# Kernel tuning notes

Measured on AMD Instinct MI355X. Metric: run time of the kernel, lower is better.

The kernel has to match this reference:

```python
import jax, jax.numpy as jnp
import numpy as np

NUM_HEADS = 32
HEAD_DIM = 128
HIDDEN = 4096
MAX_SEQ = 4096
B, S = 8, 16
POS = 2048


def setup_inputs() -> dict:
    key = jax.random.key(0)
    ks = jax.random.split(key, 7)
    sc = 1.0 / np.sqrt(HIDDEN)
    return {
        "h": jax.random.normal(ks[0], (B, S, HIDDEN), dtype=jnp.float32),
        "Wq": jax.random.normal(ks[1], (HIDDEN, HIDDEN), dtype=jnp.float32) * sc,
        "Wk": jax.random.normal(ks[2], (HIDDEN, HIDDEN), dtype=jnp.float32) * sc,
        "Wv": jax.random.normal(ks[3], (HIDDEN, HIDDEN), dtype=jnp.float32) * sc,
        "Wo": jax.random.normal(ks[4], (HIDDEN, HIDDEN), dtype=jnp.float32) * sc,
        "K_cache": jax.random.normal(ks[5], (B, NUM_HEADS, MAX_SEQ, HEAD_DIM), dtype=jnp.float32),
        "V_cache": jax.random.normal(ks[6], (B, NUM_HEADS, MAX_SEQ, HEAD_DIM), dtype=jnp.float32),
        "pos": POS,
    }


def reference(h, Wq, Wk, Wv, Wo, K_cache, V_cache, pos):
    b, s, _ = h.shape
    # QKV projections (Linear with weight [out, in], no bias): h @ W.T
    def proj(W):
        return (h @ W.T).reshape(b, s, NUM_HEADS, HEAD_DIM).transpose(0, 2, 1, 3)  # [B,H,S,hd]
    Q, K, V = proj(Wq), proj(Wk), proj(Wv)
    # write new K/V into cache at [pos : pos+S] (pos is a static Python int)
    K_cache = K_cache.at[:, :, pos:pos + s, :].set(K)
    V_cache = V_cache.at[:, :, pos:pos + s, :].set(V)
    K_all = K_cache[:, :, :pos + s, :]  # [B,H,T,hd], T = pos+S
    V_all = V_cache[:, :, :pos + s, :]
    scores = jnp.einsum('bhsd,bhtd->bhst', Q, K_all) / np.sqrt(HEAD_DIM)  # [B,H,S,T]
    if s > 1:
        # causal mask applied only to the freshly-written block of columns
        causal = jnp.triu(jnp.full((s, s), -jnp.inf, dtype=scores.dtype), k=1)
        scores = scores.at[:, :, :, pos:pos + s].add(causal)
    attn = jax.nn.softmax(scores, axis=-1)
    out = jnp.einsum('bhst,bhtd->bhsd', attn, V_all)  # [B,H,S,hd]
    out = out.transpose(0, 2, 1, 3).reshape(b, s, NUM_HEADS * HEAD_DIM)
    return out @ Wo.T
```

## Files before the change

kernel.cpp:

```cpp
#include <hip/hip_runtime.h>

typedef _Float16 f16;
typedef _Float16 f16x8 __attribute__((ext_vector_type(8)));
typedef _Float16 f16x4 __attribute__((ext_vector_type(4)));
typedef _Float16 f16x2 __attribute__((ext_vector_type(2)));
typedef float f32x4 __attribute__((ext_vector_type(4)));
typedef float f32x2 __attribute__((ext_vector_type(2)));

#define MFMA16(a, b, c) __builtin_amdgcn_mfma_f32_16x16x32_f16(a, b, c, 0, 0, 0)

#define HID 4096
#define ROWS 128
#define SCL 0.12751743f

__device__ __forceinline__ f16x8 cvt8(float4 x, float4 y) {
    f16x8 v = {(f16)x.x, (f16)x.y, (f16)x.z, (f16)x.w,
               (f16)y.x, (f16)y.y, (f16)y.z, (f16)y.w};
    return v;
}

__device__ __forceinline__ int swz2(int row, int cb) {
    return row * 256 + (cb ^ ((row & 7) << 4));
}

__global__ void k_cvt(const float* __restrict__ src, f16* __restrict__ dst) {
    const int i = blockIdx.x * blockDim.x + threadIdx.x;
    const float4* s4 = (const float4*)src + (size_t)i * 2;
    float4 x = s4[0], y = s4[1];
    *((f16x8*)dst + i) = cvt8(x, y);
}

__global__ __launch_bounds__(256) void k_proj(
        const f16* __restrict__ hb,
        const float* __restrict__ Wq, const float* __restrict__ Wk,
        const float* __restrict__ Wv,
        f16* __restrict__ Qw, f16* __restrict__ Kw, f16* __restrict__ Vw) {
    const int mat = blockIdx.x >> 8;
    const int ct  = blockIdx.x & 255;
    const float* __restrict__ W = (mat == 0) ? Wq : (mat == 1) ? Wk : Wv;
    f16* __restrict__ Ob = (mat == 0) ? Qw : (mat == 1) ? Kw : Vw;
    const int c0 = ct * 16;

    __shared__ __align__(16) f16 sA[128 * 128];
    __shared__ __align__(16) f16 sB[16 * 128];

    const int tid = threadIdx.x;
    const int w = tid >> 6, l = tid & 63;
    const int rw = w * 32;
    const int ar = tid >> 4;
    const int ac = (tid & 15) * 8;

    f32x4 acc0 = {}, acc1 = {};

    float4 wx, wy;
    f16x8 hreg[8];
    {
        const float* wp = W + (size_t)(c0 + ar) * HID + ac;
        wx = *(const float4*)wp; wy = *(const float4*)(wp + 4);
        #pragma unroll
        for (int c = 0; c < 8; ++c)
            hreg[c] = *(const f16x8*)(hb + (size_t)(c * 16 + ar) * HID + ac);
    }

    for (int ks = 0; ks < 32; ++ks) {
        #pragma unroll
        for (int c = 0; c < 8; ++c)
            *(f16x8*)((char*)sA + swz2(c * 16 + ar, ac * 2)) = hreg[c];
        *(f16x8*)((char*)sB + swz2(ar, ac * 2)) = cvt8(wx, wy);
        __syncthreads();
        if (ks < 31) {
            const int k0 = (ks + 1) * 128;
            const float* wp = W + (size_t)(c0 + ar) * HID + k0 + ac;
            wx = *(const float4*)wp; wy = *(const float4*)(wp + 4);
            #pragma unroll
            for (int c = 0; c < 8; ++c)
                hreg[c] = *(const f16x8*)(hb + (size_t)(c * 16 + ar) * HID + k0 + ac);
        }
        #pragma unroll
        for (int kk = 0; kk < 4; ++kk) {
            const int cb = kk * 64 + (l >> 4) * 16;
            f16x8 a0 = *(const f16x8*)((char*)sA + swz2(rw + (l & 15), cb));
            f16x8 a1 = *(const f16x8*)((char*)sA + swz2(rw + 16 + (l & 15), cb));
            f16x8 b0 = *(const f16x8*)((char*)sB + swz2((l & 15), cb));
            acc0 = MFMA16(a0, b0, acc0);
            acc1 = MFMA16(a1, b0, acc1);
        }
        __syncthreads();
    }
    #pragma unroll
    for (int r = 0; r < 4; ++r) {
        const int col = c0 + (l & 15);
        Ob[(size_t)(rw + (l >> 4) * 4 + r) * HID + col]      = (f16)acc0[r];
        Ob[(size_t)(rw + 16 + (l >> 4) * 4 + r) * HID + col] = (f16)acc1[r];
    }
}

__global__ __launch_bounds__(512) void k_attn(
        const f16* __restrict__ Qw, const f16* __restrict__ Kw,
        const f16* __restrict__ Vw,
        const float* __restrict__ Kc, const float* __restrict__ Vc,
        const int* __restrict__ posp, f16* __restrict__ Ow) {

    __shared__ __align__(16) char smem[65536 + 1024];

    const int bh = blockIdx.x;
    const int b = bh >> 5, hh = bh & 31;
    const int tid = threadIdx.x, w = tid >> 6, l = tid & 63;
    const int pos = *posp;
    const int npure = pos >> 5;

    const float* Kb = Kc + (size_t)bh * (4096 * 128);
    const float* Vb = Vc + (size_t)bh * (4096 * 128);

    f16x8 qf[4];
    {
        const f16* qp = Qw + (size_t)(b * 16 + (l & 15)) * HID + hh * 128 + (l >> 4) * 8;
        #pragma unroll
        for (int kk = 0; kk < 4; ++kk) qf[kk] = *(const f16x8*)(qp + kk * 32);
    }

    f32x4 o[8] = {};
    float m[4], lsum[4];
    #pragma unroll
    for (int r = 0; r < 4; ++r) { m[r] = -3e38f; lsum[r] = 0.f; }

    f16* Pw = (f16*)smem + w * 640;

    const int start = (w * npure) >> 3;
    const int end   = ((w + 1) * npure) >> 3;
    for (int tau = start; tau < end; ++tau) {
        const int t0 = tau << 5;

        f16x8 kf[2][4];
        #pragma unroll
        for (int tn = 0; tn < 2; ++tn) {
            const float* kp = Kb + (size_t)(t0 + tn * 16 + (l & 15)) * 128 + (l >> 4) * 8;
            #pragma unroll
            for (int kk = 0; kk < 4; ++kk) {
                float4 x = *(const float4*)(kp + kk * 32);
                float4 y = *(const float4*)(kp + kk * 32 + 4);
                kf[tn][kk] = cvt8(x, y);
            }
        }
        f32x4 sa[2] = {};
        #pragma unroll
        for (int tn = 0; tn < 2; ++tn)
            #pragma unroll
            for (int kk = 0; kk < 4; ++kk) sa[tn] = MFMA16(qf[kk], kf[tn][kk], sa[tn]);

        f16x8 vf[8];
        {
            const float* vp = Vb + (size_t)(t0 + (l >> 4) * 8) * 128 + (l & 15);
            #pragma unroll
            for (int dt = 0; dt < 8; ++dt)
                #pragma unroll
                for (int j = 0; j < 8; ++j) vf[dt][j] = (f16)vp[j * 128 + dt * 16];
        }

        float sc[2][4];
        #pragma unroll
        for (int tn = 0; tn < 2; ++tn)
            #pragma unroll
            for (int r = 0; r < 4; ++r) sc[tn][r] = sa[tn][r] * SCL;
        float vmax[4];
        #pragma unroll
        for (int r = 0; r < 4; ++r) vmax[r] = fmaxf(sc[0][r], sc[1][r]);
        #pragma unroll
        for (int d = 1; d < 16; d <<= 1)
            #pragma unroll
            for (int r = 0; r < 4; ++r) vmax[r] = fmaxf(vmax[r], __shfl_xor(vmax[r], d));
        float p[2][4], rs[4], fac[4];
        #pragma unroll
        for (int r = 0; r < 4; ++r) {
            const float mn = fmaxf(m[r], vmax[r]);
            fac[r] = exp2f(m[r] - mn);
            m[r] = mn;
            p[0][r] = exp2f(sc[0][r] - mn);
            p[1][r] = exp2f(sc[1][r] - mn);
            rs[r] = p[0][r] + p[1][r];
            lsum[r] *= fac[r];
        }
        #pragma unroll
        for (int d = 1; d < 16; d <<= 1)
            #pragma unroll
            for (int r = 0; r < 4; ++r) rs[r] += __shfl_xor(rs[r], d);
        #pragma unroll
        for (int r = 0; r < 4; ++r) lsum[r] += rs[r];
        #pragma unroll
        for (int dt = 0; dt < 8; ++dt)
            #pragma unroll
            for (int r = 0; r < 4; ++r) o[dt][r] *= fac[r];

        #pragma unroll
        for (int r = 0; r < 4; ++r) {
            const int s_ = (l >> 4) * 4 + r;
            Pw[s_ * 40 + (l & 15)]      = (f16)p[0][r];
            Pw[s_ * 40 + 16 + (l & 15)] = (f16)p[1][r];
        }
        asm volatile("s_waitcnt lgkmcnt(0)" ::: "memory");
        f16x8 pa = *(const f16x8*)(Pw + (l & 15) * 40 + (l >> 4) * 8);

        #pragma unroll
        for (int dt = 0; dt < 8; ++dt) o[dt] = MFMA16(pa, vf[dt], o[dt]);
    }

    if (w == 7) {
        for (int t0 = npure << 5; t0 < pos + 16; t0 += 32) {
            f32x4 sa[2] = {};
            bool tnv[2];
            #pragma unroll
            for (int tn = 0; tn < 2; ++tn) {
                tnv[tn] = (t0 + tn * 16 < pos + 16);
                if (!tnv[tn]) continue;
                const int trow = t0 + tn * 16 + (l & 15);
                f16x8 kf[4];
                if (trow < pos) {
                    const float* kp = Kb + (size_t)trow * 128 + (l >> 4) * 8;
                    #pragma unroll
                    for (int kk = 0; kk < 4; ++kk) {
                        float4 x = *(const float4*)(kp + kk * 32);
                        float4 y = *(const float4*)(kp + kk * 32 + 4);
                        kf[kk] = cvt8(x, y);
                    }
                } else {
                    const int tt = trow - pos;
                    const int rr = tt < 15 ? tt : 15;
                    const f16* kp = Kw + (size_t)(b * 16 + rr) * HID + hh * 128 + (l >> 4) * 8;
                    #pragma unroll
                    for (int kk = 0; kk < 4; ++kk) kf[kk] = *(const f16x8*)(kp + kk * 32);
                }
                #pragma unroll
                for (int kk = 0; kk < 4; ++kk) sa[tn] = MFMA16(qf[kk], kf[kk], sa[tn]);
            }

            float sc[2][4];
            #pragma unroll
            for (int tn = 0; tn < 2; ++tn) {
                const int tg = t0 + tn * 16 + (l & 15);
                #pragma unroll
                for (int r = 0; r < 4; ++r) {
                    if (!tnv[tn]) { sc[tn][r] = -3e38f; continue; }
                    float v = sa[tn][r] * SCL;
                    if (tg >= pos) {
                        const int tt = tg - pos;
                        const int s_ = (l >> 4) * 4 + r;
                        if (tt > s_ || tt >= 16) v = -3e38f;
                    }
                    sc[tn][r] = v;
                }
            }

            float vmax[4];
            #pragma unroll
            for (int r = 0; r < 4; ++r) vmax[r] = fmaxf(sc[0][r], sc[1][r]);
            #pragma unroll
            for (int d = 1; d < 16; d <<= 1)
                #pragma unroll
                for (int r = 0; r < 4; ++r) vmax[r] = fmaxf(vmax[r], __shfl_xor(vmax[r], d));
            float p[2][4], rs[4], fac[4];
            #pragma unroll
            for (int r = 0; r < 4; ++r) {
                const float mn = fmaxf(m[r], vmax[r]);
                fac[r] = exp2f(m[r] - mn);
                m[r] = mn;
                p[0][r] = sc[0][r] < -1e29f ? 0.f : exp2f(sc[0][r] - mn);
                p[1][r] = sc[1][r] < -1e29f ? 0.f : exp2f(sc[1][r] - mn);
                rs[r] = p[0][r] + p[1][r];
                lsum[r] *= fac[r];
            }
            #pragma unroll
            for (int d = 1; d < 16; d <<= 1)
                #pragma unroll
                for (int r = 0; r < 4; ++r) rs[r] += __shfl_xor(rs[r], d);
            #pragma unroll
            for (int r = 0; r < 4; ++r) lsum[r] += rs[r];
            #pragma unroll
            for (int dt = 0; dt < 8; ++dt)
                #pragma unroll
                for (int r = 0; r < 4; ++r) o[dt][r] *= fac[r];

            #pragma unroll
            for (int r = 0; r < 4; ++r) {
                const int s_ = (l >> 4) * 4 + r;
                Pw[s_ * 40 + (l & 15)]      = (f16)p[0][r];
                Pw[s_ * 40 + 16 + (l & 15)] = (f16)p[1][r];
            }
            asm volatile("s_waitcnt lgkmcnt(0)" ::: "memory");
            f16x8 pa = *(const f16x8*)(Pw + (l & 15) * 40 + (l >> 4) * 8);

            const int tb = t0 + (l >> 4) * 8;
            #pragma unroll
            for (int dt = 0; dt < 8; ++dt) {
                f16x8 vf;
                #pragma unroll
                for (int j = 0; j < 8; ++j) {
                    const int t = tb + j;
                    if (t < pos) {
                        vf[j] = (f16)Vb[(size_t)t * 128 + dt * 16 + (l & 15)];
                    } else {
                        const int rr = (t - pos < 15) ? (t - pos) : 15;
                        vf[j] = Vw[(size_t)(b * 16 + rr) * HID + hh * 128 + dt * 16 + (l & 15)];
                    }
                }
                o[dt] = MFMA16(pa, vf, o[dt]);
            }
        }
    }

    __syncthreads();
    float* Osh = (float*)smem;
    float* Msh = (float*)(smem + 65536);
    float* Lsh = Msh + 128;
    #pragma unroll
    for (int dt = 0; dt < 8; ++dt)
        #pragma unroll
        for (int r = 0; r < 4; ++r)
            Osh[w * 2048 + ((l >> 4) * 4 + r) * 128 + dt * 16 + (l & 15)] = o[dt][r];
    if ((l & 15) == 0) {
        #pragma unroll
        for (int r = 0; r < 4; ++r) {
            Msh[w * 16 + (l >> 4) * 4 + r] = m[r];
            Lsh[w * 16 + (l >> 4) * 4 + r] = lsum[r];
        }
    }
    __syncthreads();
    {
        const int s_ = tid >> 5;
        const int d_ = (tid & 31) * 4;
        float M = -3e38f;
        #pragma unroll
        for (int ww = 0; ww < 8; ++ww) M = fmaxf(M, Msh[ww * 16 + s_]);
        float L = 0.f;
        f32x4 oa = {};
        #pragma unroll
        for (int ww = 0; ww < 8; ++ww) {
            const float e = exp2f(Msh[ww * 16 + s_] - M);
            L += e * Lsh[ww * 16 + s_];
            f32x4 v = *(const f32x4*)(Osh + ww * 2048 + s_ * 128 + d_);
            #pragma unroll
            for (int r = 0; r < 4; ++r) oa[r] += e * v[r];
        }
        const float inv = 1.f / L;
        f16x4 res = {(f16)(oa[0] * inv), (f16)(oa[1] * inv),
                     (f16)(oa[2] * inv), (f16)(oa[3] * inv)};
        *(f16x4*)(Ow + (size_t)(b * 16 + s_) * HID + hh * 128 + d_) = res;
    }
}

__global__ __launch_bounds__(256) void k_oproj(
        const f16* __restrict__ Oa, const float* __restrict__ Wo,
        float* __restrict__ out) {
    const int c0 = blockIdx.x * 16;

    __shared__ __align__(16) f16 sA[128 * 128];
    __shared__ __align__(16) f16 sB[16 * 128];

    const int tid = threadIdx.x;
    const int w = tid >> 6, l = tid & 63;
    const int rw = w * 32;
    const int ar = tid >> 4;
    const int ac = (tid & 15) * 8;

    f32x4 acc0 = {}, acc1 = {};

    float4 wx, wy;
    f16x8 hreg[8];
    {
        const float* wp = Wo + (size_t)(c0 + ar) * HID + ac;
        wx = *(const float4*)wp; wy = *(const float4*)(wp + 4);
        #pragma unroll
        for (int c = 0; c < 8; ++c)
            hreg[c] = *(const f16x8*)(Oa + (size_t)(c * 16 + ar) * HID + ac);
    }

    for (int ks = 0; ks < 32; ++ks) {
        #pragma unroll
        for (int c = 0; c < 8; ++c)
            *(f16x8*)((char*)sA + swz2(c * 16 + ar, ac * 2)) = hreg[c];
        *(f16x8*)((char*)sB + swz2(ar, ac * 2)) = cvt8(wx, wy);
        __syncthreads();
        if (ks < 31) {
            const int k0 = (ks + 1) * 128;
            const float* wp = Wo + (size_t)(c0 + ar) * HID + k0 + ac;
            wx = *(const float4*)wp; wy = *(const float4*)(wp + 4);
            #pragma unroll
            for (int c = 0; c < 8; ++c)
                hreg[c] = *(const f16x8*)(Oa + (size_t)(c * 16 + ar) * HID + k0 + ac);
        }
        #pragma unroll
        for (int kk = 0; kk < 4; ++kk) {
            const int cb = kk * 64 + (l >> 4) * 16;
            f16x8 a0 = *(const f16x8*)((char*)sA + swz2(rw + (l & 15), cb));
            f16x8 a1 = *(const f16x8*)((char*)sA + swz2(rw + 16 + (l & 15), cb));
            f16x8 b0 = *(const f16x8*)((char*)sB + swz2((l & 15), cb));
            acc0 = MFMA16(a0, b0, acc0);
            acc1 = MFMA16(a1, b0, acc1);
        }
        __syncthreads();
    }
    #pragma unroll
    for (int r = 0; r < 4; ++r) {
        const int col = c0 + (l & 15);
        out[(size_t)(rw + (l >> 4) * 4 + r) * HID + col]      = acc0[r];
        out[(size_t)(rw + 16 + (l >> 4) * 4 + r) * HID + col] = acc1[r];
    }
}

extern "C" void kernel_launch(void* const* d_in, const int* in_sizes, int n_in,
                              void* d_out, int out_size, void* d_ws, size_t ws_size,
                              hipStream_t stream) {
    const float* h  = (const float*)d_in[0];
    const float* Wq = (const float*)d_in[1];
    const float* Wk = (const float*)d_in[2];
    const float* Wv = (const float*)d_in[3];
    const float* Wo = (const float*)d_in[4];
    const float* Kc = (const float*)d_in[5];
    const float* Vc = (const float*)d_in[6];
    const int* pos  = (const int*)d_in[7];
    float* out = (float*)d_out;

    f16* hws = (f16*)d_ws;
    f16* Qw  = hws + ROWS * HID;
    f16* Kw  = Qw + ROWS * HID;
    f16* Vw  = Kw + ROWS * HID;
    f16* Ow  = Vw + ROWS * HID;

    k_cvt<<<256, 256, 0, stream>>>(h, hws);
    k_proj<<<768, 256, 0, stream>>>(hws, Wq, Wk, Wv, Qw, Kw, Vw);
    k_attn<<<256, 512, 0, stream>>>(Qw, Kw, Vw, Kc, Vc, pos, Ow);
    k_oproj<<<256, 256, 0, stream>>>(Ow, Wo, out);
}
```

Before: 205.6 us.

## Overlap K/V projection with cached-prefix attention in one interleaved kernel

The Q projection now runs on its own. The K and V projections are merged into one launch with the attention over the pure cached prefix: odd blocks do the K/V GEMM and even blocks compute partial softmax state (max, sum, output) for each head. A new finalize kernel then handles the tail block, including the newly written K/V rows, with the causal mask, and merges it with the partial results. This is meant to hide the long cache-streaming attention behind the projection GEMM and to remove the slow single-wave tail loop. The cost is an extra launch and a round trip of the partial results through global memory.

```diff
diff --git a/kernel.cpp b/kernel.cpp
--- a/kernel.cpp
+++ b/kernel.cpp
@@ -30,16 +30,10 @@
     *((f16x8*)dst + i) = cvt8(x, y);
 }
 
-__global__ __launch_bounds__(256) void k_proj(
-        const f16* __restrict__ hb,
-        const float* __restrict__ Wq, const float* __restrict__ Wk,
-        const float* __restrict__ Wv,
-        f16* __restrict__ Qw, f16* __restrict__ Kw, f16* __restrict__ Vw) {
-    const int mat = blockIdx.x >> 8;
-    const int ct  = blockIdx.x & 255;
-    const float* __restrict__ W = (mat == 0) ? Wq : (mat == 1) ? Wk : Wv;
-    f16* __restrict__ Ob = (mat == 0) ? Qw : (mat == 1) ? Kw : Vw;
-    const int c0 = ct * 16;
+__global__ __launch_bounds__(256) void k_qproj(
+        const f16* __restrict__ hb, const float* __restrict__ W,
+        f16* __restrict__ Ob) {
+    const int c0 = blockIdx.x * 16;
 
     __shared__ __align__(16) f16 sA[128 * 128];
     __shared__ __align__(16) f16 sB[16 * 128];
@@ -95,17 +89,81 @@
     }
 }
 
-__global__ __launch_bounds__(512) void k_attn(
-        const f16* __restrict__ Qw, const f16* __restrict__ Kw,
-        const f16* __restrict__ Vw,
+__global__ __launch_bounds__(512) void k_mega(
+        const f16* __restrict__ hb,
+        const float* __restrict__ Wk, const float* __restrict__ Wv,
+        f16* __restrict__ Kw, f16* __restrict__ Vw,
+        const f16* __restrict__ Qw,
         const float* __restrict__ Kc, const float* __restrict__ Vc,
-        const int* __restrict__ posp, f16* __restrict__ Ow) {
+        const int* __restrict__ posp,
+        float* __restrict__ Pm, float* __restrict__ Pl, float* __restrict__ Po) {
 
     __shared__ __align__(16) char smem[65536 + 1024];
-
-    const int bh = blockIdx.x;
+    const int tid = threadIdx.x, w = tid >> 6, l = tid & 63;
+
+    if (blockIdx.x & 1) {
+        const int pid = blockIdx.x >> 1;
+        const float* __restrict__ W = (pid & 128) ? Wv : Wk;
+        f16* __restrict__ Ob = (pid & 128) ? Vw : Kw;
+        const int c0 = (pid & 127) * 32;
+
+        f16* sA = (f16*)smem;
+        f16* sB = (f16*)smem + 128 * 128;
+
+        const int ar = tid >> 4;
+        const int ac = (tid & 15) * 8;
+
+        f32x4 acc0 = {}, acc1 = {};
+
+        float4 wx, wy;
+        f16x8 hreg[4];
+        {
+            const float* wp = W + (size_t)(c0 + ar) * HID + ac;
+            wx = *(const float4*)wp; wy = *(const float4*)(wp + 4);
+            #pragma unroll
+            for (int c = 0; c < 4; ++c)
+                hreg[c] = *(const f16x8*)(hb + (size_t)(c * 32 + ar) * HID + ac);
+        }
+
+        const int rw = (w >> 1) * 32;
+        const int cw = (w & 1) * 16;
+
+        for (int ks = 0; ks < 32; ++ks) {
+            #pragma unroll
+            for (int c = 0; c < 4; ++c)
+                *(f16x8*)((char*)sA + swz2(c * 32 + ar, ac * 2)) = hreg[c];
+            *(f16x8*)((char*)sB + swz2(ar, ac * 2)) = cvt8(wx, wy);
+            __syncthreads();
+            if (ks < 31) {
+                const int k0 = (ks + 1) * 128;
+                const float* wp = W + (size_t)(c0 + ar) * HID + k0 + ac;
+                wx = *(const float4*)wp; wy = *(const float4*)(wp + 4);
+                #pragma unroll
+                for (int c = 0; c < 4; ++c)
+                    hreg[c] = *(const f16x8*)(hb + (size_t)(c * 32 + ar) * HID + k0 + ac);
+            }
+            #pragma unroll
+            for (int kk = 0; kk < 4; ++kk) {
+                const int cb = kk * 64 + (l >> 4) * 16;
+                f16x8 a0 = *(const f16x8*)((char*)sA + swz2(rw + (l & 15), cb));
+                f16x8 a1 = *(const f16x8*)((char*)sA + swz2(rw + 16 + (l & 15), cb));
+                f16x8 b0 = *(const f16x8*)((char*)sB + swz2(cw + (l & 15), cb));
+                acc0 = MFMA16(a0, b0, acc0);
+                acc1 = MFMA16(a1, b0, acc1);
+            }
+            __syncthreads();
+        }
+        #pragma unroll
+        for (int r = 0; r < 4; ++r) {
+            const int col = c0 + cw + (l & 15);
+            Ob[(size_t)(rw + (l >> 4) * 4 + r) * HID + col]      = (f16)acc0[r];
+            Ob[(size_t)(rw + 16 + (l >> 4) * 4 + r) * HID + col] = (f16)acc1[r];
+        }
+        return;
+    }
+
+    const int bh = blockIdx.x >> 1;
     const int b = bh >> 5, hh = bh & 31;
-    const int tid = threadIdx.x, w = tid >> 6, l = tid & 63;
     const int pos = *posp;
     const int npure = pos >> 5;
 
@@ -204,109 +262,6 @@
         for (int dt = 0; dt < 8; ++dt) o[dt] = MFMA16(pa, vf[dt], o[dt]);
     }
 
-    if (w == 7) {
-        for (int t0 = npure << 5; t0 < pos + 16; t0 += 32) {
-            f32x4 sa[2] = {};
-            bool tnv[2];
-            #pragma unroll
-            for (int tn = 0; tn < 2; ++tn) {
-                tnv[tn] = (t0 + tn * 16 < pos + 16);
-                if (!tnv[tn]) continue;
-                const int trow = t0 + tn * 16 + (l & 15);
-                f16x8 kf[4];
-                if (trow < pos) {
-                    const float* kp = Kb + (size_t)trow * 128 + (l >> 4) * 8;
-                    #pragma unroll
-                    for (int kk = 0; kk < 4; ++kk) {
-                        float4 x = *(const float4*)(kp + kk * 32);
-                        float4 y = *(const float4*)(kp + kk * 32 + 4);
-                        kf[kk] = cvt8(x, y);
-                    }
-                } else {
-                    const int tt = trow - pos;
-                    const int rr = tt < 15 ? tt : 15;
-                    const f16* kp = Kw + (size_t)(b * 16 + rr) * HID + hh * 128 + (l >> 4) * 8;
-                    #pragma unroll
-                    for (int kk = 0; kk < 4; ++kk) kf[kk] = *(const f16x8*)(kp + kk * 32);
-                }
-                #pragma unroll
-                for (int kk = 0; kk < 4; ++kk) sa[tn] = MFMA16(qf[kk], kf[kk], sa[tn]);
-            }
-
-            float sc[2][4];
-            #pragma unroll
-            for (int tn = 0; tn < 2; ++tn) {
-                const int tg = t0 + tn * 16 + (l & 15);
-                #pragma unroll
-                for (int r = 0; r < 4; ++r) {
-                    if (!tnv[tn]) { sc[tn][r] = -3e38f; continue; }
-                    float v = sa[tn][r] * SCL;
-                    if (tg >= pos) {
-                        const int tt = tg - pos;
-                        const int s_ = (l >> 4) * 4 + r;
-                        if (tt > s_ || tt >= 16) v = -3e38f;
-                    }
-                    sc[tn][r] = v;
-                }
-            }
-
-            float vmax[4];
-            #pragma unroll
-            for (int r = 0; r < 4; ++r) vmax[r] = fmaxf(sc[0][r], sc[1][r]);
-            #pragma unroll
-            for (int d = 1; d < 16; d <<= 1)
-                #pragma unroll
-                for (int r = 0; r < 4; ++r) vmax[r] = fmaxf(vmax[r], __shfl_xor(vmax[r], d));
-            float p[2][4], rs[4], fac[4];
-            #pragma unroll
-            for (int r = 0; r < 4; ++r) {
-                const float mn = fmaxf(m[r], vmax[r]);
-                fac[r] = exp2f(m[r] - mn);
-                m[r] = mn;
-                p[0][r] = sc[0][r] < -1e29f ? 0.f : exp2f(sc[0][r] - mn);
-                p[1][r] = sc[1][r] < -1e29f ? 0.f : exp2f(sc[1][r] - mn);
-                rs[r] = p[0][r] + p[1][r];
-                lsum[r] *= fac[r];
-            }
-            #pragma unroll
-            for (int d = 1; d < 16; d <<= 1)
-                #pragma unroll
-                for (int r = 0; r < 4; ++r) rs[r] += __shfl_xor(rs[r], d);
-            #pragma unroll
-            for (int r = 0; r < 4; ++r) lsum[r] += rs[r];
-            #pragma unroll
-            for (int dt = 0; dt < 8; ++dt)
-                #pragma unroll
-                for (int r = 0; r < 4; ++r) o[dt][r] *= fac[r];
-
-            #pragma unroll
-            for (int r = 0; r < 4; ++r) {
-                const int s_ = (l >> 4) * 4 + r;
-                Pw[s_ * 40 + (l & 15)]      = (f16)p[0][r];
-                Pw[s_ * 40 + 16 + (l & 15)] = (f16)p[1][r];
-            }
-            asm volatile("s_waitcnt lgkmcnt(0)" ::: "memory");
-            f16x8 pa = *(const f16x8*)(Pw + (l & 15) * 40 + (l >> 4) * 8);
-
-            const int tb = t0 + (l >> 4) * 8;
-            #pragma unroll
-            for (int dt = 0; dt < 8; ++dt) {
-                f16x8 vf;
-                #pragma unroll
-                for (int j = 0; j < 8; ++j) {
-                    const int t = tb + j;
-                    if (t < pos) {
-                        vf[j] = (f16)Vb[(size_t)t * 128 + dt * 16 + (l & 15)];
-                    } else {
-                        const int rr = (t - pos < 15) ? (t - pos) : 15;
-                        vf[j] = Vw[(size_t)(b * 16 + rr) * HID + hh * 128 + dt * 16 + (l & 15)];
-                    }
-                }
-                o[dt] = MFMA16(pa, vf, o[dt]);
-            }
-        }
-    }
-
     __syncthreads();
     float* Osh = (float*)smem;
     float* Msh = (float*)(smem + 65536);
@@ -340,10 +295,129 @@
             #pragma unroll
             for (int r = 0; r < 4; ++r) oa[r] += e * v[r];
         }
-        const float inv = 1.f / L;
-        f16x4 res = {(f16)(oa[0] * inv), (f16)(oa[1] * inv),
-                     (f16)(oa[2] * inv), (f16)(oa[3] * inv)};
-        *(f16x4*)(Ow + (size_t)(b * 16 + s_) * HID + hh * 128 + d_) = res;
+        if ((tid & 31) == 0) {
+            Pm[bh * 16 + s_] = M;
+            Pl[bh * 16 + s_] = L;
+        }
+        *(f32x4*)(Po + (size_t)bh * 2048 + s_ * 128 + d_) = oa;
+    }
+}
+
+__global__ __launch_bounds__(256) void k_fin(
+        const f16* __restrict__ Qw, const f16* __restrict__ Kw,
+        const f16* __restrict__ Vw,
+        const float* __restrict__ Kc, const float* __restrict__ Vc,
+        const int* __restrict__ posp,
+        const float* __restrict__ Pm, const float* __restrict__ Pl,
+        const float* __restrict__ Po, f16* __restrict__ Ow) {
+
+    __shared__ float sP[16][48];
+    __shared__ float sF[16], sL[16];
+
+    const int bh = blockIdx.x, b = bh >> 5, hh = bh & 31;
+    const int tid = threadIdx.x;
+    const int pos = *posp;
+    const int base = (pos >> 5) << 5;
+    const int nb = pos + 16 - base;
+
+    {
+        const int s_ = tid >> 4, tt0 = tid & 15;
+        const f16* qp = Qw + (size_t)(b * 16 + s_) * HID + hh * 128;
+        const float m_p = Pm[bh * 16 + s_];
+        const float l_p = Pl[bh * 16 + s_];
+
+        float sc[3];
+        float rowmax = -3e38f;
+        #pragma unroll
+        for (int it = 0; it < 3; ++it) {
+            const int tt = it * 16 + tt0;
+            float d = -3e38f;
+            if (tt < nb) {
+                const int t = base + tt;
+                float acc = 0.f;
+                if (t < pos) {
+                    const float* kp = Kc + ((size_t)bh * 4096 + t) * 128;
+                    #pragma unroll
+                    for (int c = 0; c < 16; ++c) {
+                        f16x8 q8 = *(const f16x8*)(qp + c * 8);
+                        float4 ka = *(const float4*)(kp + c * 8);
+                        float4 kb = *(const float4*)(kp + c * 8 + 4);
+                        acc += (float)q8[0] * ka.x + (float)q8[1] * ka.y +
+                               (float)q8[2] * ka.z + (float)q8[3] * ka.w +
+                               (float)q8[4] * kb.x + (float)q8[5] * kb.y +
+                               (float)q8[6] * kb.z + (float)q8[7] * kb.w;
+                    }
+                    d = acc * SCL;
+                } else {
+                    const f16* kp = Kw + (size_t)(b * 16 + (t - pos)) * HID + hh * 128;
+                    #pragma unroll
+                    for (int c = 0; c < 16; ++c) {
+                        f16x8 q8 = *(const f16x8*)(qp + c * 8);
+                        f16x8 k8 = *(const f16x8*)(kp + c * 8);
+                        #pragma unroll
+                        for (int j = 0; j < 8; ++j) acc += (float)q8[j] * (float)k8[j];
+                    }
+                    d = acc * SCL;
+                    if ((t - pos) > s_) d = -3e38f;
+                }
+            }
+            sc[it] = d;
+            rowmax = fmaxf(rowmax, d);
+        }
+        #pragma unroll
+        for (int dd = 1; dd < 16; dd <<= 1)
+            rowmax = fmaxf(rowmax, __shfl_xor(rowmax, dd));
+
+        const float M = fmaxf(m_p, rowmax);
+        const float fac = exp2f(m_p - M);
+        float ps = 0.f;
+        #pragma unroll
+        for (int it = 0; it < 3; ++it) {
+            const float p = (sc[it] < -1e29f) ? 0.f : exp2f(sc[it] - M);
+            ps += p;
+            sP[s_][it * 16 + tt0] = p;
+        }
+        #pragma unroll
+        for (int dd = 1; dd < 16; dd <<= 1) ps += __shfl_xor(ps, dd);
+        if (tt0 == 0) {
+            sF[s_] = fac;
+            sL[s_] = fac * l_p + ps;
+        }
+    }
+    __syncthreads();
+
+    {
+        const int s2 = tid >> 4;
+        const int d0 = (tid & 15) * 8;
+        const float f = sF[s2];
+        float acc[8];
+        const float* po = Po + (size_t)bh * 2048 + s2 * 128 + d0;
+        #pragma unroll
+        for (int j = 0; j < 8; ++j) acc[j] = f * po[j];
+
+        for (int tt = 0; tt < nb; ++tt) {
+            const float pv = sP[s2][tt];
+            const int t = base + tt;
+            if (t < pos) {
+                const float* vp = Vc + ((size_t)bh * 4096 + t) * 128 + d0;
+                float4 va = *(const float4*)vp;
+                float4 vb = *(const float4*)(vp + 4);
+                acc[0] += pv * va.x; acc[1] += pv * va.y;
+                acc[2] += pv * va.z; acc[3] += pv * va.w;
+                acc[4] += pv * vb.x; acc[5] += pv * vb.y;
+                acc[6] += pv * vb.z; acc[7] += pv * vb.w;
+            } else {
+                const f16* vp = Vw + (size_t)(b * 16 + (t - pos)) * HID + hh * 128 + d0;
+                f16x8 v8 = *(const f16x8*)vp;
+                #pragma unroll
+                for (int j = 0; j < 8; ++j) acc[j] += pv * (float)v8[j];
+            }
+        }
+        const float inv = 1.f / sL[s2];
+        f16x8 res;
+        #pragma unroll
+        for (int j = 0; j < 8; ++j) res[j] = (f16)(acc[j] * inv);
+        *(f16x8*)(Ow + (size_t)(b * 16 + s2) * HID + hh * 128 + d0) = res;
     }
 }
 
@@ -424,9 +498,13 @@
     f16* Kw  = Qw + ROWS * HID;
     f16* Vw  = Kw + ROWS * HID;
     f16* Ow  = Vw + ROWS * HID;
+    float* Pm = (float*)(Ow + ROWS * HID);
+    float* Pl = Pm + 256 * 16;
+    float* Po = Pl + 256 * 16;
 
     k_cvt<<<256, 256, 0, stream>>>(h, hws);
-    k_proj<<<768, 256, 0, stream>>>(hws, Wq, Wk, Wv, Qw, Kw, Vw);
-    k_attn<<<256, 512, 0, stream>>>(Qw, Kw, Vw, Kc, Vc, pos, Ow);
+    k_qproj<<<256, 256, 0, stream>>>(hws, Wq, Qw);
+    k_mega<<<512, 512, 0, stream>>>(hws, Wk, Wv, Kw, Vw, Qw, Kc, Vc, pos, Pm, Pl, Po);
+    k_fin<<<256, 256, 0, stream>>>(Qw, Kw, Vw, Kc, Vc, pos, Pm, Pl, Po, Ow);
     k_oproj<<<256, 256, 0, stream>>>(Ow, Wo, out);
 }
```

Measured after the change: 229.1 us. 1.11x slower.

## Load projection MFMA operands directly from global memory, dropping LDS staging

Applied to the files above, without the earlier changes.

The QKV projection kernel no longer stages the activation and weight tiles through shared memory with swizzling and two barriers per k-step. Each lane now loads its MFMA operand fragments straight from global memory into registers, double-buffered across k-steps, and converts weights to fp16 in registers. Launch bounds now request 3 blocks per CU. This removes LDS traffic and synchronization, but each of the four waves independently reloads the same 16-column weight slice, and the per-lane global loads are strided rather than fully coalesced.

```diff
diff --git a/kernel.cpp b/kernel.cpp
--- a/kernel.cpp
+++ b/kernel.cpp
@@ -30,7 +30,7 @@
     *((f16x8*)dst + i) = cvt8(x, y);
 }
 
-__global__ __launch_bounds__(256) void k_proj(
+__global__ __launch_bounds__(256, 3) void k_proj(
         const f16* __restrict__ hb,
         const float* __restrict__ Wq, const float* __restrict__ Wk,
         const float* __restrict__ Wv,
@@ -41,57 +41,61 @@
     f16* __restrict__ Ob = (mat == 0) ? Qw : (mat == 1) ? Kw : Vw;
     const int c0 = ct * 16;
 
-    __shared__ __align__(16) f16 sA[128 * 128];
-    __shared__ __align__(16) f16 sB[16 * 128];
-
     const int tid = threadIdx.x;
     const int w = tid >> 6, l = tid & 63;
-    const int rw = w * 32;
-    const int ar = tid >> 4;
-    const int ac = (tid & 15) * 8;
+    const int r0 = w * 32;
+
+    const float* wp  = W  + (size_t)(c0 + (l & 15)) * HID + ((l >> 4) * 8);
+    const f16*   hp0 = hb + (size_t)(r0 + (l & 15)) * HID + ((l >> 4) * 8);
+    const f16*   hp1 = hp0 + (size_t)16 * HID;
 
     f32x4 acc0 = {}, acc1 = {};
 
-    float4 wx, wy;
-    f16x8 hreg[8];
-    {
-        const float* wp = W + (size_t)(c0 + ar) * HID + ac;
-        wx = *(const float4*)wp; wy = *(const float4*)(wp + 4);
-        #pragma unroll
-        for (int c = 0; c < 8; ++c)
-            hreg[c] = *(const f16x8*)(hb + (size_t)(c * 16 + ar) * HID + ac);
+    float4 wf[4][2];
+    f16x8  ha[2][4];
+
+    #pragma unroll
+    for (int kk = 0; kk < 4; ++kk) {
+        wf[kk][0] = *(const float4*)(wp + kk * 32);
+        wf[kk][1] = *(const float4*)(wp + kk * 32 + 4);
+        ha[0][kk] = *(const f16x8*)(hp0 + kk * 32);
+        ha[1][kk] = *(const f16x8*)(hp1 + kk * 32);
     }
 
     for (int ks = 0; ks < 32; ++ks) {
-        #pragma unroll
-        for (int c = 0; c < 8; ++c)
-            *(f16x8*)((char*)sA + swz2(c * 16 + ar, ac * 2)) = hreg[c];
-        *(f16x8*)((char*)sB + swz2(ar, ac * 2)) = cvt8(wx, wy);
-        __syncthreads();
+        float4 nwf[4][2];
+        f16x8  nha[2][4];
         if (ks < 31) {
             const int k0 = (ks + 1) * 128;
-            const float* wp = W + (size_t)(c0 + ar) * HID + k0 + ac;
-            wx = *(const float4*)wp; wy = *(const float4*)(wp + 4);
-            #pragma unroll
-            for (int c = 0; c < 8; ++c)
-                hreg[c] = *(const f16x8*)(hb + (size_t)(c * 16 + ar) * HID + k0 + ac);
+            #pragma unroll
+            for (int kk = 0; kk < 4; ++kk) {
+                nwf[kk][0] = *(const float4*)(wp + k0 + kk * 32);
+                nwf[kk][1] = *(const float4*)(wp + k0 + kk * 32 + 4);
+                nha[0][kk] = *(const f16x8*)(hp0 + k0 + kk * 32);
+                nha[1][kk] = *(const f16x8*)(hp1 + k0 + kk * 32);
+            }
         }
         #pragma unroll
         for (int kk = 0; kk < 4; ++kk) {
-            const int cb = kk * 64 + (l >> 4) * 16;
-            f16x8 a0 = *(const f16x8*)((char*)sA + swz2(rw + (l & 15), cb));
-            f16x8 a1 = *(const f16x8*)((char*)sA + swz2(rw + 16 + (l & 15), cb));
-            f16x8 b0 = *(const f16x8*)((char*)sB + swz2((l & 15), cb));
-            acc0 = MFMA16(a0, b0, acc0);
-            acc1 = MFMA16(a1, b0, acc1);
-        }
-        __syncthreads();
-    }
+            const f16x8 bw = cvt8(wf[kk][0], wf[kk][1]);
+            acc0 = MFMA16(ha[0][kk], bw, acc0);
+            acc1 = MFMA16(ha[1][kk], bw, acc1);
+        }
+        if (ks < 31) {
+            #pragma unroll
+            for (int kk = 0; kk < 4; ++kk) {
+                wf[kk][0] = nwf[kk][0]; wf[kk][1] = nwf[kk][1];
+                ha[0][kk] = nha[0][kk]; ha[1][kk] = nha[1][kk];
+            }
+        }
+    }
+
     #pragma unroll
     for (int r = 0; r < 4; ++r) {
+        const int row = r0 + (l >> 4) * 4 + r;
         const int col = c0 + (l & 15);
-        Ob[(size_t)(rw + (l >> 4) * 4 + r) * HID + col]      = (f16)acc0[r];
-        Ob[(size_t)(rw + 16 + (l >> 4) * 4 + r) * HID + col] = (f16)acc1[r];
+        Ob[(size_t)row * HID + col]        = (f16)acc0[r];
+        Ob[(size_t)(row + 16) * HID + col] = (f16)acc1[r];
     }
 }
 
```

New measurement: 310.3 us. +50.9%, slower.

## Split QKV projection K dimension in two and sum partials in attention

Applied to the files above, without the earlier changes.

The QKV projection now uses split-K: each output tile is computed by two blocks over halves of the reduction dimension, so the grid doubles to 1536 blocks. The partial results are stored in fp32 and the attention kernel adds the two halves when it loads Q, the new K and the new V. This is meant to improve occupancy and latency hiding in the projection GEMM, which had few blocks per CU. In exchange it doubles the fp32 partial-output traffic to the workspace and adds extra loads in the attention kernel.

```diff
diff --git a/kernel.cpp b/kernel.cpp
--- a/kernel.cpp
+++ b/kernel.cpp
@@ -3,19 +3,26 @@
 typedef _Float16 f16;
 typedef _Float16 f16x8 __attribute__((ext_vector_type(8)));
 typedef _Float16 f16x4 __attribute__((ext_vector_type(4)));
-typedef _Float16 f16x2 __attribute__((ext_vector_type(2)));
 typedef float f32x4 __attribute__((ext_vector_type(4)));
-typedef float f32x2 __attribute__((ext_vector_type(2)));
 
 #define MFMA16(a, b, c) __builtin_amdgcn_mfma_f32_16x16x32_f16(a, b, c, 0, 0, 0)
 
 #define HID 4096
 #define ROWS 128
+#define PH (ROWS * HID)
 #define SCL 0.12751743f
 
 __device__ __forceinline__ f16x8 cvt8(float4 x, float4 y) {
     f16x8 v = {(f16)x.x, (f16)x.y, (f16)x.z, (f16)x.w,
                (f16)y.x, (f16)y.y, (f16)y.z, (f16)y.w};
+    return v;
+}
+
+__device__ __forceinline__ f16x8 cvt8s(float4 x0, float4 x1, float4 y0, float4 y1) {
+    f16x8 v = {(f16)(x0.x + x1.x), (f16)(x0.y + x1.y),
+               (f16)(x0.z + x1.z), (f16)(x0.w + x1.w),
+               (f16)(y0.x + y1.x), (f16)(y0.y + y1.y),
+               (f16)(y0.z + y1.z), (f16)(y0.w + y1.w)};
     return v;
 }
 
@@ -34,12 +41,14 @@
         const f16* __restrict__ hb,
         const float* __restrict__ Wq, const float* __restrict__ Wk,
         const float* __restrict__ Wv,
-        f16* __restrict__ Qw, f16* __restrict__ Kw, f16* __restrict__ Vw) {
-    const int mat = blockIdx.x >> 8;
-    const int ct  = blockIdx.x & 255;
+        float* __restrict__ Qp, float* __restrict__ Kp, float* __restrict__ Vp) {
+    const int half = blockIdx.x & 1;
+    const int ct   = (blockIdx.x >> 1) & 255;
+    const int mat  = blockIdx.x >> 9;
     const float* __restrict__ W = (mat == 0) ? Wq : (mat == 1) ? Wk : Wv;
-    f16* __restrict__ Ob = (mat == 0) ? Qw : (mat == 1) ? Kw : Vw;
-    const int c0 = ct * 16;
+    float* __restrict__ Pb = ((mat == 0) ? Qp : (mat == 1) ? Kp : Vp) + (size_t)half * PH;
+    const int c0  = ct * 16;
+    const int k00 = half * 2048;
 
     __shared__ __align__(16) f16 sA[128 * 128];
     __shared__ __align__(16) f16 sB[16 * 128];
@@ -55,21 +64,21 @@
     float4 wx, wy;
     f16x8 hreg[8];
     {
-        const float* wp = W + (size_t)(c0 + ar) * HID + ac;
+        const float* wp = W + (size_t)(c0 + ar) * HID + k00 + ac;
         wx = *(const float4*)wp; wy = *(const float4*)(wp + 4);
         #pragma unroll
         for (int c = 0; c < 8; ++c)
-            hreg[c] = *(const f16x8*)(hb + (size_t)(c * 16 + ar) * HID + ac);
-    }
-
-    for (int ks = 0; ks < 32; ++ks) {
+            hreg[c] = *(const f16x8*)(hb + (size_t)(c * 16 + ar) * HID + k00 + ac);
+    }
+
+    for (int ks = 0; ks < 16; ++ks) {
         #pragma unroll
         for (int c = 0; c < 8; ++c)
             *(f16x8*)((char*)sA + swz2(c * 16 + ar, ac * 2)) = hreg[c];
         *(f16x8*)((char*)sB + swz2(ar, ac * 2)) = cvt8(wx, wy);
         __syncthreads();
-        if (ks < 31) {
-            const int k0 = (ks + 1) * 128;
+        if (ks < 15) {
+            const int k0 = k00 + (ks + 1) * 128;
             const float* wp = W + (size_t)(c0 + ar) * HID + k0 + ac;
             wx = *(const float4*)wp; wy = *(const float4*)(wp + 4);
             #pragma unroll
@@ -90,14 +99,14 @@
     #pragma unroll
     for (int r = 0; r < 4; ++r) {
         const int col = c0 + (l & 15);
-        Ob[(size_t)(rw + (l >> 4) * 4 + r) * HID + col]      = (f16)acc0[r];
-        Ob[(size_t)(rw + 16 + (l >> 4) * 4 + r) * HID + col] = (f16)acc1[r];
+        Pb[(size_t)(rw + (l >> 4) * 4 + r) * HID + col]      = acc0[r];
+        Pb[(size_t)(rw + 16 + (l >> 4) * 4 + r) * HID + col] = acc1[r];
     }
 }
 
 __global__ __launch_bounds__(512) void k_attn(
-        const f16* __restrict__ Qw, const f16* __restrict__ Kw,
-        const f16* __restrict__ Vw,
+        const float* __restrict__ Qp, const float* __restrict__ Kp,
+        const float* __restrict__ Vp,
         const float* __restrict__ Kc, const float* __restrict__ Vc,
         const int* __restrict__ posp, f16* __restrict__ Ow) {
 
@@ -114,9 +123,12 @@
 
     f16x8 qf[4];
     {
-        const f16* qp = Qw + (size_t)(b * 16 + (l & 15)) * HID + hh * 128 + (l >> 4) * 8;
-        #pragma unroll
-        for (int kk = 0; kk < 4; ++kk) qf[kk] = *(const f16x8*)(qp + kk * 32);
+        const float* q0 = Qp + (size_t)(b * 16 + (l & 15)) * HID + hh * 128 + (l >> 4) * 8;
+        const float* q1 = q0 + PH;
+        #pragma unroll
+        for (int kk = 0; kk < 4; ++kk)
+            qf[kk] = cvt8s(*(const float4*)(q0 + kk * 32),     *(const float4*)(q1 + kk * 32),
+                           *(const float4*)(q0 + kk * 32 + 4), *(const float4*)(q1 + kk * 32 + 4));
     }
 
     f32x4 o[8] = {};
@@ -225,9 +237,12 @@
                 } else {
                     const int tt = trow - pos;
                     const int rr = tt < 15 ? tt : 15;
-                    const f16* kp = Kw + (size_t)(b * 16 + rr) * HID + hh * 128 + (l >> 4) * 8;
+                    const float* k0 = Kp + (size_t)(b * 16 + rr) * HID + hh * 128 + (l >> 4) * 8;
+                    const float* k1 = k0 + PH;
                     #pragma unroll
-                    for (int kk = 0; kk < 4; ++kk) kf[kk] = *(const f16x8*)(kp + kk * 32);
+                    for (int kk = 0; kk < 4; ++kk)
+                        kf[kk] = cvt8s(*(const float4*)(k0 + kk * 32),     *(const float4*)(k1 + kk * 32),
+                                       *(const float4*)(k0 + kk * 32 + 4), *(const float4*)(k1 + kk * 32 + 4));
                 }
                 #pragma unroll
                 for (int kk = 0; kk < 4; ++kk) sa[tn] = MFMA16(qf[kk], kf[kk], sa[tn]);
@@ -299,7 +314,8 @@
                         vf[j] = (f16)Vb[(size_t)t * 128 + dt * 16 + (l & 15)];
                     } else {
                         const int rr = (t - pos < 15) ? (t - pos) : 15;
-                        vf[j] = Vw[(size_t)(b * 16 + rr) * HID + hh * 128 + dt * 16 + (l & 15)];
+                        const size_t off = (size_t)(b * 16 + rr) * HID + hh * 128 + dt * 16 + (l & 15);
+                        vf[j] = (f16)(Vp[off] + Vp[off + PH]);
                     }
                 }
                 o[dt] = MFMA16(pa, vf, o[dt]);
@@ -419,14 +435,14 @@
     const int* pos  = (const int*)d_in[7];
     float* out = (float*)d_out;
 
-    f16* hws = (f16*)d_ws;
-    f16* Qw  = hws + ROWS * HID;
-    f16* Kw  = Qw + ROWS * HID;
-    f16* Vw  = Kw + ROWS * HID;
-    f16* Ow  = Vw + ROWS * HID;
+    f16* hws  = (f16*)d_ws;
+    float* Qp = (float*)(hws + ROWS * HID);
+    float* Kp = Qp + 2 * PH;
+    float* Vp = Kp + 2 * PH;
+    f16* Ow   = (f16*)(Vp + 2 * PH);
 
     k_cvt<<<256, 256, 0, stream>>>(h, hws);
-    k_proj<<<768, 256, 0, stream>>>(hws, Wq, Wk, Wv, Qw, Kw, Vw);
-    k_attn<<<256, 512, 0, stream>>>(Qw, Kw, Vw, Kc, Vc, pos, Ow);
+    k_proj<<<1536, 256, 0, stream>>>(hws, Wq, Wk, Wv, Qp, Kp, Vp);
+    k_attn<<<256, 512, 0, stream>>>(Qp, Kp, Vp, Kc, Vc, pos, Ow);
     k_oproj<<<256, 256, 0, stream>>>(Ow, Wo, out);
 }
```

Result: slower. 221.1 us (+7.5%).
